# Kernel tuning notes

Hardware: AMD Instinct MI355X
Metric: run time of the kernel (lower is better)

The kernel has to match this reference:

```python
import jax, jax.numpy as jnp
import numpy as np

D_MODEL, D_LOW, NUM_BINS = 512, 64, 39
DIST_MIN, DIST_MAX = 2.0, 22.0
BIN_WIDTH = (DIST_MAX - DIST_MIN) / (NUM_BINS - 1)
LN_EPS = 1e-5


def setup_inputs() -> dict:
    key = jax.random.key(0)
    ks = jax.random.split(key, 10)
    B, N = 2, 768
    h_res = jax.random.normal(ks[0], (B, N, D_MODEL), dtype=jnp.float32)
    # scale coords so pairwise distances span the [2, 22] bin range
    x_true = jax.random.normal(ks[1], (B, N, 3), dtype=jnp.float32) * 5.0
    token_pad_mask = jnp.ones((B, N), dtype=jnp.float32)
    s = 1.0 / np.sqrt(D_MODEL)
    return {
        "h_res": h_res,
        "x_true": x_true,
        "token_pad_mask": token_pad_mask,
        "ln_w": jnp.ones((D_MODEL,), jnp.float32),
        "ln_b": jnp.zeros((D_MODEL,), jnp.float32),
        "wu_w": jax.random.normal(ks[2], (D_LOW, D_MODEL), jnp.float32) * s,
        "wu_b": jnp.zeros((D_LOW,), jnp.float32),
        "wv_w": jax.random.normal(ks[3], (D_LOW, D_MODEL), jnp.float32) * s,
        "wv_b": jnp.zeros((D_LOW,), jnp.float32),
        "wb_w": jax.random.normal(ks[4], (NUM_BINS, D_LOW), jnp.float32) * (1.0 / np.sqrt(D_LOW)),
        "wb_b": jnp.zeros((NUM_BINS,), jnp.float32),
    }


def _layernorm(x, w, b):
    mu = jnp.mean(x, axis=-1, keepdims=True)
    var = jnp.mean(jnp.square(x - mu), axis=-1, keepdims=True)
    return (x - mu) * jax.lax.rsqrt(var + LN_EPS) * w + b


def reference(h_res, x_true, token_pad_mask, ln_w, ln_b, wu_w, wu_b, wv_w, wv_b, wb_w, wb_b):
    B, N, _ = h_res.shape
    # pairwise distances -> target bins (trunc-to-int then clamp, as torch .long())
    diff = x_true[:, :, None, :] - x_true[:, None, :, :]          # [B,N,N,3]
    d_true = jnp.sqrt(jnp.sum(diff * diff, axis=-1))               # [B,N,N]
    target = jnp.clip(((d_true - DIST_MIN) / BIN_WIDTH).astype(jnp.int32), 0, NUM_BINS - 1)

    h = _layernorm(h_res, ln_w, ln_b)
    U = h @ wu_w.T + wu_b                                          # [B,N,d_low]
    V = h @ wv_w.T + wv_b                                          # [B,N,d_low]
    # logits[b,i,j,k] = sum_c U[b,i,c] V[b,j,c] Wb[k,c] + bb[k]
    logits = jnp.einsum("bic,bjc,kc->bijk", U, V, wb_w) + wb_b     # [B,N,N,K]
    logp = jax.nn.log_softmax(logits, axis=-1)
    ce = -jnp.take_along_axis(logp, target[..., None], axis=-1)[..., 0]  # [B,N,N]

    mask = (token_pad_mask[:, :, None] * token_pad_mask[:, None, :]) > 0  # [B,N,N] bool
    counts = jnp.sum(mask, axis=(1, 2))                            # [B]
    per_sample = jnp.sum(jnp.where(mask, ce, 0.0), axis=(1, 2)) / jnp.maximum(counts, 1)
    valid = counts > 0
    total_count = jnp.sum(valid)
    loss = jnp.sum(jnp.where(valid, per_sample, 0.0)) / jnp.maximum(total_count, 1)
    return loss
```

## Files before the change

kernel.cpp:

```cpp
#include <hip/hip_runtime.h>
#include <hip/hip_bf16.h>
#include <math.h>

#define D_MODEL 512
#define D_LOW   64
#define NBINS   39
#define LOG2E   1.4426950408889634f
#define LN2     0.6931471805599453f

typedef __attribute__((ext_vector_type(8))) short short8;
typedef __attribute__((ext_vector_type(4))) float floatx4;

__global__ __launch_bounds__(256) void prep_kernel(
    const float* __restrict__ ln_w, const float* __restrict__ ln_b,
    const float* __restrict__ wu_w, const float* __restrict__ wu_b,
    const float* __restrict__ wv_w, const float* __restrict__ wv_b,
    const float* __restrict__ wb_b,
    __hip_bfloat16* __restrict__ w2bf, float* __restrict__ w2sum,
    float* __restrict__ b2, float* __restrict__ bb2) {
  __shared__ float red[8];
  const int o   = blockIdx.x;
  const int tid = threadIdx.x;
  const bool isU = (o < 64);
  const float* wrow = isU ? (wu_w + o * D_MODEL) : (wv_w + (o - 64) * D_MODEL);
  const float scale = isU ? LOG2E : 1.0f;

  float s1 = 0.f, s2 = 0.f;
  for (int c = tid; c < D_MODEL; c += 256) {
    const float w  = wrow[c];
    const float w2 = w * ln_w[c] * scale;
    const __hip_bfloat16 hb = __float2bfloat16(w2);
    w2bf[o * D_MODEL + c] = hb;
    s1 += __bfloat162float(hb);
    s2 += w * ln_b[c];
  }
  #pragma unroll
  for (int off = 32; off; off >>= 1) {
    s1 += __shfl_xor(s1, off);
    s2 += __shfl_xor(s2, off);
  }
  const int wave = tid >> 6, lane = tid & 63;
  if (lane == 0) { red[wave] = s1; red[4 + wave] = s2; }
  __syncthreads();
  if (tid == 0) {
    w2sum[o] = red[0] + red[1] + red[2] + red[3];
    const float ss2 = red[4] + red[5] + red[6] + red[7];
    b2[o] = scale * ((isU ? wu_b[o] : wv_b[o - 64]) + ss2);
  }
  if (o == 0 && tid < 48)
    bb2[tid] = (tid < NBINS) ? LOG2E * wb_b[tid] : -INFINITY;
}

__global__ __launch_bounds__(256) void lnproj_mfma_kernel(
    const float* __restrict__ h_res, const __hip_bfloat16* __restrict__ w2bf,
    const float* __restrict__ w2sum, const float* __restrict__ b2,
    float* __restrict__ U, __hip_bfloat16* __restrict__ Vbf, int N) {
  const int tid  = threadIdx.x;
  const int wave = tid >> 6, lane = tid & 63;
  const int q = lane >> 4, ln16 = lane & 15;
  const int row0 = blockIdx.x * 16;
  const float* hp = h_res + (size_t)(row0 + ln16) * D_MODEL + q * 8;

  short8 abf[16];
  float sum = 0.f, ssq = 0.f;
  #pragma unroll
  for (int kc = 0; kc < 16; ++kc) {
    const floatx4 x0 = *reinterpret_cast<const floatx4*>(hp + kc * 32);
    const floatx4 x1 = *reinterpret_cast<const floatx4*>(hp + kc * 32 + 4);
    short8 a;
    #pragma unroll
    for (int e = 0; e < 4; ++e) {
      sum += x0[e]; ssq += x0[e] * x0[e];
      const __hip_bfloat16 hb = __float2bfloat16(x0[e]);
      a[e] = *reinterpret_cast<const short*>(&hb);
    }
    #pragma unroll
    for (int e = 0; e < 4; ++e) {
      sum += x1[e]; ssq += x1[e] * x1[e];
      const __hip_bfloat16 hb = __float2bfloat16(x1[e]);
      a[4 + e] = *reinterpret_cast<const short*>(&hb);
    }
    abf[kc] = a;
  }
  sum += __shfl_xor(sum, 16); sum += __shfl_xor(sum, 32);
  ssq += __shfl_xor(ssq, 16); ssq += __shfl_xor(ssq, 32);
  const float mu  = sum * (1.0f / (float)D_MODEL);
  const float var = ssq * (1.0f / (float)D_MODEL) - mu * mu;
  const float rs  = rsqrtf(var + 1e-5f);
  float mu_r[4], rs_r[4];
  #pragma unroll
  for (int r = 0; r < 4; ++r) {
    mu_r[r] = __shfl(mu, q * 4 + r);
    rs_r[r] = __shfl(rs, q * 4 + r);
  }

  const int obase = wave * 32;
  const short* wp = reinterpret_cast<const short*>(w2bf);
  floatx4 acc0 = (floatx4){0.f, 0.f, 0.f, 0.f};
  floatx4 acc1 = (floatx4){0.f, 0.f, 0.f, 0.f};
  #pragma unroll
  for (int kc = 0; kc < 16; ++kc) {
    const short8 b0 = *reinterpret_cast<const short8*>(
        wp + (size_t)(obase + ln16) * D_MODEL + kc * 32 + q * 8);
    const short8 b1 = *reinterpret_cast<const short8*>(
        wp + (size_t)(obase + 16 + ln16) * D_MODEL + kc * 32 + q * 8);
    acc0 = __builtin_amdgcn_mfma_f32_16x16x32_bf16(abf[kc], b0, acc0, 0, 0, 0);
    acc1 = __builtin_amdgcn_mfma_f32_16x16x32_bf16(abf[kc], b1, acc1, 0, 0, 0);
  }

  #pragma unroll
  for (int nt = 0; nt < 2; ++nt) {
    const int out = obase + nt * 16 + ln16;
    const floatx4 a = nt ? acc1 : acc0;
    const float ws = w2sum[out];
    const float bb = b2[out];
    #pragma unroll
    for (int r = 0; r < 4; ++r) {
      const int rowg = row0 + q * 4 + r;
      const float val = rs_r[r] * a[r] - mu_r[r] * rs_r[r] * ws + bb;
      if (out < 64) {
        U[(size_t)rowg * D_LOW + out] = val;
      } else {
        Vbf[(size_t)rowg * D_LOW + (out - 64)] = __float2bfloat16(val);
      }
    }
  }
}

__global__ __launch_bounds__(256) void pair_mfma_kernel(
    const float* __restrict__ U,
    const __hip_bfloat16* __restrict__ Vbf,
    const float* __restrict__ x_true, const float* __restrict__ pmask,
    const float* __restrict__ wb_w, const float* __restrict__ bb2,
    float* __restrict__ part, int N) {
  __shared__ int tbm[768];
  __shared__ float rbuf[8];
  const int i = blockIdx.x, b = blockIdx.y;
  const int tid  = threadIdx.x;
  const int wave = tid >> 6, lane = tid & 63;
  const int q = lane >> 4, ln16 = lane & 15;
  const int rowi = b * N + i;

  const float xi0 = x_true[rowi * 3 + 0];
  const float xi1 = x_true[rowi * 3 + 1];
  const float xi2 = x_true[rowi * 3 + 2];
  const float pmi = pmask[rowi];
  const float BW  = (22.0f - 2.0f) / 38.0f;
  for (int j = tid; j < N; j += 256) {
    const int rowj = b * N + j;
    const float dx = xi0 - x_true[rowj * 3 + 0];
    const float dy = xi1 - x_true[rowj * 3 + 1];
    const float dz = xi2 - x_true[rowj * 3 + 2];
    const float d  = sqrtf(dx * dx + dy * dy + dz * dz);
    int tb = (int)((d - 2.0f) / BW);
    tb = tb < 0 ? 0 : (tb > NBINS - 1 ? NBINS - 1 : tb);
    tbm[j] = (pmi * pmask[rowj] > 0.f) ? tb : -1;
  }

  short8 wfrag[3][2];
  {
    const float* Up = U + (size_t)rowi * D_LOW;
    #pragma unroll
    for (int t = 0; t < 3; ++t) {
      const int n = t * 16 + ln16;
      #pragma unroll
      for (int s = 0; s < 2; ++s) {
        const int c0 = s * 32 + q * 8;
        short8 f;
        #pragma unroll
        for (int e = 0; e < 8; ++e) {
          const float w = (n < NBINS) ? wb_w[n * D_LOW + c0 + e] : 0.f;
          const float v = Up[c0 + e] * w;
          const __hip_bfloat16 hb = __float2bfloat16(v);
          f[e] = *reinterpret_cast<const short*>(&hb);
        }
        wfrag[t][s] = f;
      }
    }
  }

  float bias2[3][4];
  #pragma unroll
  for (int t = 0; t < 3; ++t)
    #pragma unroll
    for (int r = 0; r < 4; ++r) bias2[t][r] = bb2[t * 16 + q * 4 + r];

  __syncthreads();

  const short* Vp = reinterpret_cast<const short*>(Vbf) + (size_t)b * N * D_LOW;
  float ce_sum = 0.f, cnt_sum = 0.f;

  for (int g = 0; g < 6; ++g) {
    const int jb = wave * 192 + g * 32;

    short8 v[2][2];
    #pragma unroll
    for (int tt = 0; tt < 2; ++tt) {
      const size_t jr = jb + tt * 16 + ln16;
      v[tt][0] = *reinterpret_cast<const short8*>(Vp + jr * D_LOW + q * 8);
      v[tt][1] = *reinterpret_cast<const short8*>(Vp + jr * D_LOW + 32 + q * 8);
    }

    floatx4 f[2][3];
    #pragma unroll
    for (int tt = 0; tt < 2; ++tt)
      #pragma unroll
      for (int t = 0; t < 3; ++t) {
        floatx4 a = (floatx4){0.f, 0.f, 0.f, 0.f};
        a = __builtin_amdgcn_mfma_f32_16x16x32_bf16(wfrag[t][0], v[tt][0], a, 0, 0, 0);
        a = __builtin_amdgcn_mfma_f32_16x16x32_bf16(wfrag[t][1], v[tt][1], a, 0, 0, 0);
        f[tt][t] = a;
      }

    #pragma unroll
    for (int tt = 0; tt < 2; ++tt) {
      const int j  = jb + tt * 16 + ln16;
      const int tb = tbm[j];
      float ssum = 0.f, lt = 0.f;
      #pragma unroll
      for (int t = 0; t < 3; ++t)
        #pragma unroll
        for (int r = 0; r < 4; ++r) {
          const float l2 = f[tt][t][r] + bias2[t][r];
          ssum += __builtin_amdgcn_exp2f(l2);
          lt += (t * 16 + q * 4 + r == tb) ? l2 : 0.f;
        }
      ssum += __shfl_xor(ssum, 16); ssum += __shfl_xor(ssum, 32);
      lt   += __shfl_xor(lt, 16);   lt   += __shfl_xor(lt, 32);
      const float ce = LN2 * (__builtin_amdgcn_logf(ssum) - lt);
      const float ok = (tb >= 0) ? 1.f : 0.f;
      ce_sum  += ok * ce;
      cnt_sum += ok;
    }
  }

  #pragma unroll
  for (int off = 32; off; off >>= 1) {
    ce_sum  += __shfl_xor(ce_sum, off);
    cnt_sum += __shfl_xor(cnt_sum, off);
  }
  if (lane == 0) { rbuf[wave] = ce_sum; rbuf[4 + wave] = cnt_sum; }
  __syncthreads();
  if (tid == 0) {
    part[rowi * 2 + 0] = rbuf[0] + rbuf[1] + rbuf[2] + rbuf[3];
    part[rowi * 2 + 1] = rbuf[4] + rbuf[5] + rbuf[6] + rbuf[7];
  }
}

__global__ __launch_bounds__(256) void finalize_kernel(
    const float* __restrict__ part, float* __restrict__ out, int N, int B) {
  __shared__ float red[8];
  const int tid = threadIdx.x, wave = tid >> 6, lane = tid & 63;
  float loss = 0.f, vcount = 0.f;
  for (int b = 0; b < B; ++b) {
    float ce = 0.f, cnt = 0.f;
    for (int i = tid; i < N; i += 256) {
      ce  += part[(b * N + i) * 2 + 0];
      cnt += part[(b * N + i) * 2 + 1];
    }
    #pragma unroll
    for (int off = 32; off; off >>= 1) {
      ce  += __shfl_xor(ce, off);
      cnt += __shfl_xor(cnt, off);
    }
    if (lane == 0) { red[wave] = ce; red[4 + wave] = cnt; }
    __syncthreads();
    if (tid == 0) {
      const float s = red[0] + red[1] + red[2] + red[3];
      const float c = red[4] + red[5] + red[6] + red[7];
      if (c > 0.f) { loss += s / fmaxf(c, 1.f); vcount += 1.f; }
    }
    __syncthreads();
  }
  if (tid == 0) out[0] = (vcount > 0.f) ? loss / vcount : 0.f;
}

extern "C" void kernel_launch(void* const* d_in, const int* in_sizes, int n_in,
                              void* d_out, int out_size, void* d_ws, size_t ws_size,
                              hipStream_t stream) {
  const float* h_res  = (const float*)d_in[0];
  const float* x_true = (const float*)d_in[1];
  const float* pmask  = (const float*)d_in[2];
  const float* ln_w   = (const float*)d_in[3];
  const float* ln_b   = (const float*)d_in[4];
  const float* wu_w   = (const float*)d_in[5];
  const float* wu_b   = (const float*)d_in[6];
  const float* wv_w   = (const float*)d_in[7];
  const float* wv_b   = (const float*)d_in[8];
  const float* wb_w   = (const float*)d_in[9];
  const float* wb_b   = (const float*)d_in[10];

  const int B  = 2;
  const int N  = in_sizes[2] / B;
  const int BN = B * N;

  float* U = (float*)d_ws;
  __hip_bfloat16* Vbf  = (__hip_bfloat16*)(U + (size_t)BN * D_LOW);
  __hip_bfloat16* w2bf = Vbf + (size_t)BN * D_LOW;
  float* w2sum = (float*)(w2bf + 128 * D_MODEL);
  float* b2    = w2sum + 128;
  float* bb2   = b2 + 128;
  float* part  = bb2 + 48;

  prep_kernel<<<128, 256, 0, stream>>>(ln_w, ln_b, wu_w, wu_b, wv_w, wv_b,
                                       wb_b, w2bf, w2sum, b2, bb2);
  lnproj_mfma_kernel<<<BN / 16, 256, 0, stream>>>(h_res, w2bf, w2sum, b2,
                                                  U, Vbf, N);
  pair_mfma_kernel<<<dim3(N, B), 256, 0, stream>>>(U, Vbf, x_true, pmask,
                                                   wb_w, bb2, part, N);
  finalize_kernel<<<1, 256, 0, stream>>>(part, (float*)d_out, N, B);
}
```

Before: 120.5 us.

## Fold weight prep into projection kernel and precompute target bins in extra blocks

```diff
diff --git a/kernel.cpp b/kernel.cpp
--- a/kernel.cpp
+++ b/kernel.cpp
@@ -11,51 +11,39 @@
 typedef __attribute__((ext_vector_type(8))) short short8;
 typedef __attribute__((ext_vector_type(4))) float floatx4;
 
-__global__ __launch_bounds__(256) void prep_kernel(
+__global__ __launch_bounds__(256) void lnproj_tbin_kernel(
+    const float* __restrict__ h_res,
     const float* __restrict__ ln_w, const float* __restrict__ ln_b,
     const float* __restrict__ wu_w, const float* __restrict__ wu_b,
     const float* __restrict__ wv_w, const float* __restrict__ wv_b,
-    const float* __restrict__ wb_b,
-    __hip_bfloat16* __restrict__ w2bf, float* __restrict__ w2sum,
-    float* __restrict__ b2, float* __restrict__ bb2) {
-  __shared__ float red[8];
-  const int o   = blockIdx.x;
+    const float* __restrict__ x_true, const float* __restrict__ pmask,
+    float* __restrict__ U, __hip_bfloat16* __restrict__ Vbf,
+    signed char* __restrict__ tbg, int N, int B, int nLN, int TB) {
   const int tid = threadIdx.x;
-  const bool isU = (o < 64);
-  const float* wrow = isU ? (wu_w + o * D_MODEL) : (wv_w + (o - 64) * D_MODEL);
-  const float scale = isU ? LOG2E : 1.0f;
-
-  float s1 = 0.f, s2 = 0.f;
-  for (int c = tid; c < D_MODEL; c += 256) {
-    const float w  = wrow[c];
-    const float w2 = w * ln_w[c] * scale;
-    const __hip_bfloat16 hb = __float2bfloat16(w2);
-    w2bf[o * D_MODEL + c] = hb;
-    s1 += __bfloat162float(hb);
-    s2 += w * ln_b[c];
-  }
-  #pragma unroll
-  for (int off = 32; off; off >>= 1) {
-    s1 += __shfl_xor(s1, off);
-    s2 += __shfl_xor(s2, off);
-  }
-  const int wave = tid >> 6, lane = tid & 63;
-  if (lane == 0) { red[wave] = s1; red[4 + wave] = s2; }
-  __syncthreads();
-  if (tid == 0) {
-    w2sum[o] = red[0] + red[1] + red[2] + red[3];
-    const float ss2 = red[4] + red[5] + red[6] + red[7];
-    b2[o] = scale * ((isU ? wu_b[o] : wv_b[o - 64]) + ss2);
-  }
-  if (o == 0 && tid < 48)
-    bb2[tid] = (tid < NBINS) ? LOG2E * wb_b[tid] : -INFINITY;
-}
-
-__global__ __launch_bounds__(256) void lnproj_mfma_kernel(
-    const float* __restrict__ h_res, const __hip_bfloat16* __restrict__ w2bf,
-    const float* __restrict__ w2sum, const float* __restrict__ b2,
-    float* __restrict__ U, __hip_bfloat16* __restrict__ Vbf, int N) {
-  const int tid  = threadIdx.x;
+
+  if ((int)blockIdx.x >= nLN) {
+    const int idx   = blockIdx.x - nLN;
+    const int NN    = N * N;
+    const int total = B * NN;
+    const float BW  = (22.0f - 2.0f) / 38.0f;
+    for (int p = idx * 256 + tid; p < total; p += TB * 256) {
+      const int b = p / NN;
+      const int r = p - b * NN;
+      const int i = r / N;
+      const int j = r - i * N;
+      const int rowi = b * N + i, rowj = b * N + j;
+      const float dx = x_true[rowi * 3 + 0] - x_true[rowj * 3 + 0];
+      const float dy = x_true[rowi * 3 + 1] - x_true[rowj * 3 + 1];
+      const float dz = x_true[rowi * 3 + 2] - x_true[rowj * 3 + 2];
+      const float d  = sqrtf(dx * dx + dy * dy + dz * dz);
+      int tb = (int)((d - 2.0f) / BW);
+      tb = tb < 0 ? 0 : (tb > NBINS - 1 ? NBINS - 1 : tb);
+      const bool ok = (pmask[rowi] * pmask[rowj]) > 0.f;
+      tbg[p] = ok ? (signed char)tb : (signed char)-1;
+    }
+    return;
+  }
+
   const int wave = tid >> 6, lane = tid & 63;
   const int q = lane >> 4, ln16 = lane & 15;
   const int row0 = blockIdx.x * 16;
@@ -95,25 +83,64 @@
   }
 
   const int obase = wave * 32;
-  const short* wp = reinterpret_cast<const short*>(w2bf);
+  const int out0 = obase + ln16;
+  const int out1 = obase + 16 + ln16;
+  const float* wr0 = (out0 < 64) ? (wu_w + out0 * D_MODEL) : (wv_w + (out0 - 64) * D_MODEL);
+  const float* wr1 = (out1 < 64) ? (wu_w + out1 * D_MODEL) : (wv_w + (out1 - 64) * D_MODEL);
+  const float sc0 = (out0 < 64) ? LOG2E : 1.0f;
+  const float sc1 = (out1 < 64) ? LOG2E : 1.0f;
+
   floatx4 acc0 = (floatx4){0.f, 0.f, 0.f, 0.f};
   floatx4 acc1 = (floatx4){0.f, 0.f, 0.f, 0.f};
+  float s1a = 0.f, s1b = 0.f;
+  float s2a = 0.f, s2b = 0.f;
   #pragma unroll
   for (int kc = 0; kc < 16; ++kc) {
-    const short8 b0 = *reinterpret_cast<const short8*>(
-        wp + (size_t)(obase + ln16) * D_MODEL + kc * 32 + q * 8);
-    const short8 b1 = *reinterpret_cast<const short8*>(
-        wp + (size_t)(obase + 16 + ln16) * D_MODEL + kc * 32 + q * 8);
+    const int c0 = kc * 32 + q * 8;
+    const floatx4 lw0 = *reinterpret_cast<const floatx4*>(ln_w + c0);
+    const floatx4 lw1 = *reinterpret_cast<const floatx4*>(ln_w + c0 + 4);
+    const floatx4 lb0 = *reinterpret_cast<const floatx4*>(ln_b + c0);
+    const floatx4 lb1 = *reinterpret_cast<const floatx4*>(ln_b + c0 + 4);
+    const floatx4 wa0 = *reinterpret_cast<const floatx4*>(wr0 + c0);
+    const floatx4 wa1 = *reinterpret_cast<const floatx4*>(wr0 + c0 + 4);
+    const floatx4 wb0 = *reinterpret_cast<const floatx4*>(wr1 + c0);
+    const floatx4 wb1 = *reinterpret_cast<const floatx4*>(wr1 + c0 + 4);
+    short8 b0, b1;
+    #pragma unroll
+    for (int e = 0; e < 4; ++e) {
+      const float v0 = wa0[e] * lw0[e] * sc0;
+      const float v1 = wa1[e] * lw1[e] * sc0;
+      const __hip_bfloat16 h0 = __float2bfloat16(v0);
+      const __hip_bfloat16 h1 = __float2bfloat16(v1);
+      b0[e]     = *reinterpret_cast<const short*>(&h0);
+      b0[4 + e] = *reinterpret_cast<const short*>(&h1);
+      s1a += __bfloat162float(h0) + __bfloat162float(h1);
+      s2a += wa0[e] * lb0[e] + wa1[e] * lb1[e];
+      const float u0 = wb0[e] * lw0[e] * sc1;
+      const float u1 = wb1[e] * lw1[e] * sc1;
+      const __hip_bfloat16 g0 = __float2bfloat16(u0);
+      const __hip_bfloat16 g1 = __float2bfloat16(u1);
+      b1[e]     = *reinterpret_cast<const short*>(&g0);
+      b1[4 + e] = *reinterpret_cast<const short*>(&g1);
+      s1b += __bfloat162float(g0) + __bfloat162float(g1);
+      s2b += wb0[e] * lb0[e] + wb1[e] * lb1[e];
+    }
     acc0 = __builtin_amdgcn_mfma_f32_16x16x32_bf16(abf[kc], b0, acc0, 0, 0, 0);
     acc1 = __builtin_amdgcn_mfma_f32_16x16x32_bf16(abf[kc], b1, acc1, 0, 0, 0);
   }
+  s1a += __shfl_xor(s1a, 16); s1a += __shfl_xor(s1a, 32);
+  s1b += __shfl_xor(s1b, 16); s1b += __shfl_xor(s1b, 32);
+  s2a += __shfl_xor(s2a, 16); s2a += __shfl_xor(s2a, 32);
+  s2b += __shfl_xor(s2b, 16); s2b += __shfl_xor(s2b, 32);
+  const float bias0 = sc0 * (((out0 < 64) ? wu_b[out0] : wv_b[out0 - 64]) + s2a);
+  const float bias1 = sc1 * (((out1 < 64) ? wu_b[out1] : wv_b[out1 - 64]) + s2b);
 
   #pragma unroll
   for (int nt = 0; nt < 2; ++nt) {
-    const int out = obase + nt * 16 + ln16;
+    const int out  = nt ? out1 : out0;
     const floatx4 a = nt ? acc1 : acc0;
-    const float ws = w2sum[out];
-    const float bb = b2[out];
+    const float ws = nt ? s1b : s1a;
+    const float bb = nt ? bias1 : bias0;
     #pragma unroll
     for (int r = 0; r < 4; ++r) {
       const int rowg = row0 + q * 4 + r;
@@ -130,32 +157,15 @@
 __global__ __launch_bounds__(256) void pair_mfma_kernel(
     const float* __restrict__ U,
     const __hip_bfloat16* __restrict__ Vbf,
-    const float* __restrict__ x_true, const float* __restrict__ pmask,
-    const float* __restrict__ wb_w, const float* __restrict__ bb2,
+    const float* __restrict__ wb_w, const float* __restrict__ wb_b,
+    const signed char* __restrict__ tbg,
     float* __restrict__ part, int N) {
-  __shared__ int tbm[768];
   __shared__ float rbuf[8];
   const int i = blockIdx.x, b = blockIdx.y;
   const int tid  = threadIdx.x;
   const int wave = tid >> 6, lane = tid & 63;
   const int q = lane >> 4, ln16 = lane & 15;
   const int rowi = b * N + i;
-
-  const float xi0 = x_true[rowi * 3 + 0];
-  const float xi1 = x_true[rowi * 3 + 1];
-  const float xi2 = x_true[rowi * 3 + 2];
-  const float pmi = pmask[rowi];
-  const float BW  = (22.0f - 2.0f) / 38.0f;
-  for (int j = tid; j < N; j += 256) {
-    const int rowj = b * N + j;
-    const float dx = xi0 - x_true[rowj * 3 + 0];
-    const float dy = xi1 - x_true[rowj * 3 + 1];
-    const float dz = xi2 - x_true[rowj * 3 + 2];
-    const float d  = sqrtf(dx * dx + dy * dy + dz * dz);
-    int tb = (int)((d - 2.0f) / BW);
-    tb = tb < 0 ? 0 : (tb > NBINS - 1 ? NBINS - 1 : tb);
-    tbm[j] = (pmi * pmask[rowj] > 0.f) ? tb : -1;
-  }
 
   short8 wfrag[3][2];
   {
@@ -183,22 +193,26 @@
   #pragma unroll
   for (int t = 0; t < 3; ++t)
     #pragma unroll
-    for (int r = 0; r < 4; ++r) bias2[t][r] = bb2[t * 16 + q * 4 + r];
-
-  __syncthreads();
+    for (int r = 0; r < 4; ++r) {
+      const int bin = t * 16 + q * 4 + r;
+      bias2[t][r] = (bin < NBINS) ? LOG2E * wb_b[bin] : -INFINITY;
+    }
 
   const short* Vp = reinterpret_cast<const short*>(Vbf) + (size_t)b * N * D_LOW;
+  const signed char* tbp = tbg + (size_t)b * N * N + (size_t)i * N;
   float ce_sum = 0.f, cnt_sum = 0.f;
 
   for (int g = 0; g < 6; ++g) {
     const int jb = wave * 192 + g * 32;
 
     short8 v[2][2];
+    int tbv[2];
     #pragma unroll
     for (int tt = 0; tt < 2; ++tt) {
       const size_t jr = jb + tt * 16 + ln16;
       v[tt][0] = *reinterpret_cast<const short8*>(Vp + jr * D_LOW + q * 8);
       v[tt][1] = *reinterpret_cast<const short8*>(Vp + jr * D_LOW + 32 + q * 8);
+      tbv[tt]  = (int)tbp[jr];
     }
 
     floatx4 f[2][3];
@@ -214,8 +228,7 @@
 
     #pragma unroll
     for (int tt = 0; tt < 2; ++tt) {
-      const int j  = jb + tt * 16 + ln16;
-      const int tb = tbm[j];
+      const int tb = tbv[tt];
       float ssum = 0.f, lt = 0.f;
       #pragma unroll
       for (int t = 0; t < 3; ++t)
@@ -226,10 +239,8 @@
           lt += (t * 16 + q * 4 + r == tb) ? l2 : 0.f;
         }
       ssum += __shfl_xor(ssum, 16); ssum += __shfl_xor(ssum, 32);
-      lt   += __shfl_xor(lt, 16);   lt   += __shfl_xor(lt, 32);
-      const float ce = LN2 * (__builtin_amdgcn_logf(ssum) - lt);
       const float ok = (tb >= 0) ? 1.f : 0.f;
-      ce_sum  += ok * ce;
+      ce_sum  += ok * LN2 * (__builtin_amdgcn_logf(ssum) - 4.0f * lt);
       cnt_sum += ok;
     }
   }
@@ -293,20 +304,18 @@
   const int B  = 2;
   const int N  = in_sizes[2] / B;
   const int BN = B * N;
+  const int nLN = BN / 16;
+  const int TB  = 160;
 
   float* U = (float*)d_ws;
-  __hip_bfloat16* Vbf  = (__hip_bfloat16*)(U + (size_t)BN * D_LOW);
-  __hip_bfloat16* w2bf = Vbf + (size_t)BN * D_LOW;
-  float* w2sum = (float*)(w2bf + 128 * D_MODEL);
-  float* b2    = w2sum + 128;
-  float* bb2   = b2 + 128;
-  float* part  = bb2 + 48;
-
-  prep_kernel<<<128, 256, 0, stream>>>(ln_w, ln_b, wu_w, wu_b, wv_w, wv_b,
-                                       wb_b, w2bf, w2sum, b2, bb2);
-  lnproj_mfma_kernel<<<BN / 16, 256, 0, stream>>>(h_res, w2bf, w2sum, b2,
-                                                  U, Vbf, N);
-  pair_mfma_kernel<<<dim3(N, B), 256, 0, stream>>>(U, Vbf, x_true, pmask,
-                                                   wb_w, bb2, part, N);
+  __hip_bfloat16* Vbf = (__hip_bfloat16*)(U + (size_t)BN * D_LOW);
+  float* part = (float*)(Vbf + (size_t)BN * D_LOW);
+  signed char* tbg = (signed char*)(part + 2 * (size_t)BN);
+
+  lnproj_tbin_kernel<<<nLN + TB, 256, 0, stream>>>(
+      h_res, ln_w, ln_b, wu_w, wu_b, wv_w, wv_b, x_true, pmask,
+      U, Vbf, tbg, N, B, nLN, TB);
+  pair_mfma_kernel<<<dim3(N, B), 256, 0, stream>>>(U, Vbf, wb_w, wb_b, tbg,
+                                                   part, N);
   finalize_kernel<<<1, 256, 0, stream>>>(part, (float*)d_out, N, B);
 }
```

Result: slower. 124.4 us (+3.2%).
